# Performance work log

Hardware: AMD Instinct MI355X
Metric: run time of the kernel (lower is better)

## Reference

```python
import jax, jax.numpy as jnp
import numpy as np

N_NODES = 20000
N_INPUT = 64
K_MAX = 12
BITS = 64
N_OUT = 10
BATCH = 64
T = 128


def setup_inputs() -> dict:
    key = jax.random.key(0)
    ks = jax.random.split(key, 8)
    x = jax.random.randint(ks[0], (BATCH, T, BITS), 0, 2, dtype=jnp.int32)
    w_in = jax.random.randint(ks[1], (BITS, N_INPUT), 0, 2, dtype=jnp.int32)
    adj_list = jax.random.randint(ks[2], (N_NODES, K_MAX), 0, N_NODES, dtype=jnp.int32)
    adj_mask = jax.random.randint(ks[3], (N_NODES, K_MAX), 0, 2, dtype=jnp.int32)
    lut = jax.random.randint(ks[4], (N_NODES, 2 ** K_MAX), 0, 2, dtype=jnp.int32)
    init_states = jax.random.randint(ks[5], (1, N_NODES), 0, 2, dtype=jnp.int32)
    W_out = jax.random.normal(ks[6], (N_OUT, N_NODES - N_INPUT), dtype=jnp.float32) * 0.02
    b_out = jnp.zeros((N_OUT,), dtype=jnp.float32)
    return {"x": x, "w_in": w_in, "adj_list": adj_list, "adj_mask": adj_mask,
            "lut": lut, "init_states": init_states, "W_out": W_out, "b_out": b_out}


def reference(x, w_in, adj_list, adj_mask, lut, init_states, W_out, b_out):
    B, T_, bits = x.shape
    N, k = adj_list.shape
    I = w_in.shape[1]
    # powers_of_2, big-endian order as in make_minimal_powers_of_two (flip)
    powers = (2 ** jnp.arange(k - 1, -1, -1)).astype(jnp.int32)  # [k]
    no_neigh = ~(adj_mask.astype(bool).any(axis=1))              # [N] nodes w/o neighbours keep state
    node_ids = jnp.arange(N)
    states0 = jnp.broadcast_to(init_states, (B, N)).astype(jnp.int32)

    def step(states, x_t):
        # inject input: bipartite mapping of input bits onto first I nodes (OR-combine)
        u = ((x_t @ w_in) > 0).astype(jnp.int32)                 # [B, I]
        states = states.at[:, :I].set(u)
        # gather incoming neighbour states per node (irregular gather)
        neigh = jnp.take(states, adj_list, axis=1)               # [B, N, k]
        neigh = neigh * adj_mask[None, :, :]
        # bit-pack into LUT index
        idx = (neigh * powers[None, None, :]).sum(axis=-1)       # [B, N], < 2^k
        new = lut[node_ids[None, :], idx]                        # [B, N] LUT lookup
        new = jnp.where(no_neigh[None, :], states, new)
        return new, None

    states, _ = jax.lax.scan(step, states0, jnp.swapaxes(x, 0, 1))
    # readout on reservoir (non-input) nodes at final timestep
    feats = states[:, I:].astype(jnp.float32)                    # [B, N-I]
    out = jax.nn.sigmoid(feats @ W_out.T + b_out)                # [B, n_outputs]
    return out
```

## Files before the change

kernel.cpp:

```cpp
#include <hip/hip_runtime.h>
#include <cstdint>
#include <cstddef>


#define N_NODES   20000
#define N_INPUT   64
#define K_MAX     12
#define T_STEPS   128
#define N_BATCH   64
#define N_OUT     10
#define N_FEAT    (N_NODES - N_INPUT)
#define DUMMY_NODE 20000
#define ST_WORDS  20004

#define NBLK 512
#define NTHR 512
#define NPB  39
#define NPB_PAD 40
#define BAR_CNT 64
#define GO_CNT  8
#define BAR_STRIDE 32

typedef unsigned long long u64;

__global__ __launch_bounds__(256) void pack_x_kernel(const int* __restrict__ x,
                                                     u64* __restrict__ xp) {
  const int t = blockIdx.x;
  const int wave = threadIdx.x >> 6, lane = threadIdx.x & 63;
  for (int b = wave; b < N_BATCH; b += 4) {
    int v = x[((size_t)b * T_STEPS + t) * 64 + lane];
    u64 bal = __ballot(v != 0);
    if (lane == 0) xp[(size_t)t * N_BATCH + b] = bal;
  }
}

__global__ __launch_bounds__(256) void init_kernel(const int* __restrict__ inis,
                                                   const int* __restrict__ w_in,
                                                   const u64* __restrict__ xp,
                                                   u64* __restrict__ buf0,
                                                   u64* __restrict__ buf1,
                                                   u64* __restrict__ wcol,
                                                   unsigned* __restrict__ bar) {
  if (blockIdx.x < 79) {
    int n = blockIdx.x * 256 + threadIdx.x;
    if (n >= N_INPUT && n < ST_WORDS) {
      u64 w = (n < N_NODES && inis[n] != 0) ? ~0ull : 0ull;
      buf0[n] = w;
      buf1[n] = w;
    }
  } else {
    const int wave = threadIdx.x >> 6, lane = threadIdx.x & 63;
    u64 xw = xp[lane];
    for (int i = wave; i < 64; i += 4) {
      int wv = w_in[(size_t)lane * 64 + i];
      u64 wc = __ballot(wv != 0);
      if (lane == 0) wcol[i] = wc;
      u64 ub = __ballot((xw & wc) != 0);
      if (lane == 0) buf0[i] = ub;
    }
    if (threadIdx.x < BAR_CNT + GO_CNT)
      bar[threadIdx.x * BAR_STRIDE] = 0u;
  }
}

__global__ __launch_bounds__(64) void u_pre_kernel(const u64* __restrict__ xp,
                                                   const u64* __restrict__ wcol,
                                                   u64* __restrict__ u_all) {
  const int t = blockIdx.x, lane = threadIdx.x;
  u64 xw = xp[(size_t)t * N_BATCH + lane];
  for (int i = 0; i < 64; i++) {
    u64 ub = __ballot((xw & wcol[i]) != 0);
    if (lane == 0) u_all[(size_t)t * 64 + i] = ub;
  }
}

__device__ __forceinline__ u64 bit_transpose64(u64 w, int lane) {
  const u64 LO0 = 0x00000000FFFFFFFFull, LO1 = 0x0000FFFF0000FFFFull,
            LO2 = 0x00FF00FF00FF00FFull, LO3 = 0x0F0F0F0F0F0F0F0Full,
            LO4 = 0x3333333333333333ull, LO5 = 0x5555555555555555ull;
#define XP_STAGE(d, LO)                                                  \
  {                                                                      \
    u64 p = (u64)__shfl_xor((long long)w, (d), 64);                      \
    if (lane & (d)) w = ((p >> (d)) & (LO)) | (w & ~(LO));               \
    else            w = (w & (LO)) | ((p << (d)) & ~(LO));               \
  }
  XP_STAGE(32, LO0) XP_STAGE(16, LO1) XP_STAGE(8, LO2)
  XP_STAGE(4,  LO3) XP_STAGE(2,  LO4) XP_STAGE(1, LO5)
#undef XP_STAGE
  return w;
}

__global__ __launch_bounds__(NTHR, 4) void reservoir_kernel(
    const int* __restrict__ lut, const int* __restrict__ adj,
    const int* __restrict__ mask, const u64* __restrict__ u_all,
    u64* __restrict__ buf0, u64* __restrict__ buf1,
    unsigned* __restrict__ bar) {
  __shared__ u64 lut_lds[NPB_PAD * 64];
  __shared__ int adj_lds[NPB_PAD * K_MAX];
  __shared__ unsigned char hn_lds[NPB_PAD];

  const int bi = blockIdx.x;
  const int tid = threadIdx.x;
  const int wave = tid >> 6, lane = tid & 63;
  const int base = N_INPUT + bi * NPB;
  const int nloc = min(NPB, N_NODES - base);

  if (tid < NPB_PAD) {
    int i = tid, h = 0;
    if (i < nloc) {
      for (int j = 0; j < K_MAX; j++) {
        int m = mask[(size_t)(base + i) * K_MAX + j];
        int a = adj[(size_t)(base + i) * K_MAX + j];
        adj_lds[i * K_MAX + (K_MAX - 1 - j)] = m ? a : DUMMY_NODE;
        h |= m;
      }
    } else {
      for (int j = 0; j < K_MAX; j++) adj_lds[i * K_MAX + j] = DUMMY_NODE;
    }
    hn_lds[i] = (unsigned char)(h ? 1 : 0);
  }

  const int nwords = nloc * 64;
  const int* lp = lut + (size_t)base * 4096;
  for (int w0 = wave * 8; w0 < nwords; w0 += 64) {
    int v[8];
#pragma unroll
    for (int q = 0; q < 8; q++) {
      int widx = w0 + q;
      v[q] = (widx < nwords) ? lp[(size_t)widx * 64 + lane] : 0;
    }
#pragma unroll
    for (int q = 0; q < 8; q++) {
      int widx = w0 + q;
      u64 bal = __ballot(v[q] != 0);
      if (lane == 0 && widx < nwords) lut_lds[widx] = bal;
    }
  }
  __syncthreads();

  const int l0 = wave * 5;
  const int cnt = min(5, nloc - l0);

  for (int t = 0; t < T_STEPS; t++) {
    u64* cur = (t & 1) ? buf1 : buf0;
    u64* nxt = (t & 1) ? buf0 : buf1;

    u64 w = 0;
    if (lane < 60) {
      int a = adj_lds[l0 * K_MAX + lane];
      w = __hip_atomic_load(&cur[a], __ATOMIC_RELAXED, __HIP_MEMORY_SCOPE_AGENT);
    }
    w = bit_transpose64(w, lane);

#pragma unroll
    for (int i = 0; i < 5; i++) {
      if (i < cnt) {
        unsigned idx = (unsigned)(w >> (12 * i)) & 0xFFFu;
        u64 g = lut_lds[(l0 + i) * 64 + (idx >> 6)];
        u64 res = __ballot((g >> (idx & 63)) & 1ull);
        if (lane == 0 && hn_lds[l0 + i])
          __hip_atomic_store(&nxt[base + l0 + i], res,
                             __ATOMIC_RELAXED, __HIP_MEMORY_SCOPE_AGENT);
      }
    }

    if (bi == NBLK - 1 && wave == 7 && t + 1 < T_STEPS) {
      u64 uw = u_all[(size_t)(t + 1) * 64 + lane];
      __hip_atomic_store(&nxt[lane], uw, __ATOMIC_RELAXED, __HIP_MEMORY_SCOPE_AGENT);
    }

    if (t != T_STEPS - 1) {
      __syncthreads();
      __builtin_amdgcn_fence(__ATOMIC_RELEASE, "workgroup");
      if (tid == 0)
        __hip_atomic_fetch_add(&bar[(bi & (BAR_CNT - 1)) * BAR_STRIDE], 1u,
                               __ATOMIC_RELAXED, __HIP_MEMORY_SCOPE_AGENT);
      if (bi == 0 && wave == 0) {
        const unsigned tgt = (unsigned)(t + 1) * (NBLK / BAR_CNT);
        for (;;) {
          unsigned c = __hip_atomic_load(&bar[lane * BAR_STRIDE],
                                         __ATOMIC_RELAXED, __HIP_MEMORY_SCOPE_AGENT);
          if (__all(c >= tgt)) break;
          __builtin_amdgcn_s_sleep(2);
        }
        if (lane < GO_CNT)
          __hip_atomic_store(&bar[(BAR_CNT + lane) * BAR_STRIDE], (unsigned)(t + 1),
                             __ATOMIC_RELAXED, __HIP_MEMORY_SCOPE_AGENT);
      } else if (wave == 0) {
        unsigned* gp = &bar[(BAR_CNT + (bi & (GO_CNT - 1))) * BAR_STRIDE];
        while (__hip_atomic_load(gp, __ATOMIC_RELAXED, __HIP_MEMORY_SCOPE_AGENT)
               < (unsigned)(t + 1))
          __builtin_amdgcn_s_sleep(2);
      }
      __builtin_amdgcn_fence(__ATOMIC_ACQUIRE, "workgroup");
      __syncthreads();
    }
  }
}

__global__ __launch_bounds__(256) void readout_kernel(const u64* __restrict__ st,
                                                      const float* __restrict__ Wout,
                                                      const float* __restrict__ bout,
                                                      float* __restrict__ out) {
  const int b = blockIdx.x / N_OUT;
  const int o = blockIdx.x % N_OUT;
  float acc = 0.f;
  for (int n = threadIdx.x; n < N_FEAT; n += 256) {
    u64 s = st[N_INPUT + n];
    float w = Wout[(size_t)o * N_FEAT + n];
    acc += ((s >> b) & 1ull) ? w : 0.f;
  }
  for (int off = 32; off > 0; off >>= 1) acc += __shfl_down(acc, off);
  __shared__ float red[4];
  const int wave = threadIdx.x >> 6, lane = threadIdx.x & 63;
  if (lane == 0) red[wave] = acc;
  __syncthreads();
  if (threadIdx.x == 0) {
    float tot = red[0] + red[1] + red[2] + red[3] + bout[o];
    out[(size_t)b * N_OUT + o] = 1.f / (1.f + __expf(-tot));
  }
}

extern "C" void kernel_launch(void* const* d_in, const int* in_sizes, int n_in,
                              void* d_out, int out_size, void* d_ws, size_t ws_size,
                              hipStream_t stream) {
  const int* x    = (const int*)d_in[0];
  const int* w_in = (const int*)d_in[1];
  const int* adj  = (const int*)d_in[2];
  const int* mask = (const int*)d_in[3];
  const int* lut  = (const int*)d_in[4];
  const int* inis = (const int*)d_in[5];
  const float* Wout = (const float*)d_in[6];
  const float* bout = (const float*)d_in[7];
  float* out = (float*)d_out;

  char* ws = (char*)d_ws;
  size_t off = 0;
  auto alloc = [&](size_t bytes) -> void* {
    void* p = ws + off;
    off += (bytes + 255) & ~(size_t)255;
    return p;
  };
  u64* buf0 = (u64*)alloc((size_t)ST_WORDS * 8);
  u64* buf1 = (u64*)alloc((size_t)ST_WORDS * 8);
  u64* xp   = (u64*)alloc((size_t)T_STEPS * N_BATCH * 8);
  u64* wcol = (u64*)alloc(64 * 8);
  u64* u_all = (u64*)alloc((size_t)T_STEPS * 64 * 8);
  unsigned* bar = (unsigned*)alloc((size_t)(BAR_CNT + GO_CNT) * BAR_STRIDE * 4);
  (void)ws_size; (void)in_sizes; (void)n_in; (void)out_size;

  hipLaunchKernelGGL(pack_x_kernel, dim3(T_STEPS), dim3(256), 0, stream, x, xp);
  hipLaunchKernelGGL(init_kernel, dim3(80), dim3(256), 0, stream,
                     inis, w_in, xp, buf0, buf1, wcol, bar);
  hipLaunchKernelGGL(u_pre_kernel, dim3(T_STEPS), dim3(64), 0, stream,
                     xp, wcol, u_all);

  void* args[] = {(void*)&lut, (void*)&adj, (void*)&mask, (void*)&u_all,
                  (void*)&buf0, (void*)&buf1, (void*)&bar};
  hipLaunchCooperativeKernel((const void*)reservoir_kernel,
                             dim3(NBLK), dim3(NTHR), args, 0, stream);

  hipLaunchKernelGGL(readout_kernel, dim3(N_BATCH * N_OUT), dim3(256), 0, stream,
                     buf0, Wout, bout, out);
}
```

Baseline: 1.033 ms.

## Use fewer, larger blocks with tree barrier and direct input-node reads

Halves the grid to 256 blocks of 1024 threads, each owning 78 nodes. The polling grid barrier, where block 0 spins on 64 counters, becomes a two-level arrival tree: the last arriver at each leaf bumps a root counter, and the last root arriver publishes the go flag. Input-node neighbours are now read straight from the precomputed per-step u_all array, so the last block no longer writes input states into the next buffer. Per-node result stores are merged into a single lane-parallel store per wave. Fewer blocks mean fewer barrier participants, at the cost of a longer serial critical path through the atomics and different occupancy with 1024-thread blocks.

```diff
diff --git a/kernel.cpp b/kernel.cpp
--- a/kernel.cpp
+++ b/kernel.cpp
@@ -13,13 +13,14 @@
 #define DUMMY_NODE 20000
 #define ST_WORDS  20004
 
-#define NBLK 512
-#define NTHR 512
-#define NPB  39
-#define NPB_PAD 40
-#define BAR_CNT 64
+#define NBLK 256
+#define NTHR 1024
+#define NPB  78
+#define NPB_PAD 80
+#define LEAF_CNT 64
 #define GO_CNT  8
 #define BAR_STRIDE 32
+#define ROOT_IDX 64
 
 typedef unsigned long long u64;
 
@@ -36,7 +37,6 @@
 
 __global__ __launch_bounds__(256) void init_kernel(const int* __restrict__ inis,
                                                    const int* __restrict__ w_in,
-                                                   const u64* __restrict__ xp,
                                                    u64* __restrict__ buf0,
                                                    u64* __restrict__ buf1,
                                                    u64* __restrict__ wcol,
@@ -50,15 +50,12 @@
     }
   } else {
     const int wave = threadIdx.x >> 6, lane = threadIdx.x & 63;
-    u64 xw = xp[lane];
     for (int i = wave; i < 64; i += 4) {
       int wv = w_in[(size_t)lane * 64 + i];
       u64 wc = __ballot(wv != 0);
       if (lane == 0) wcol[i] = wc;
-      u64 ub = __ballot((xw & wc) != 0);
-      if (lane == 0) buf0[i] = ub;
-    }
-    if (threadIdx.x < BAR_CNT + GO_CNT)
+    }
+    if (threadIdx.x < ROOT_IDX + 1 + GO_CNT)
       bar[threadIdx.x * BAR_STRIDE] = 0u;
   }
 }
@@ -90,7 +87,7 @@
   return w;
 }
 
-__global__ __launch_bounds__(NTHR, 4) void reservoir_kernel(
+__global__ __launch_bounds__(NTHR) void reservoir_kernel(
     const int* __restrict__ lut, const int* __restrict__ adj,
     const int* __restrict__ mask, const u64* __restrict__ u_all,
     u64* __restrict__ buf0, u64* __restrict__ buf1,
@@ -122,7 +119,7 @@
 
   const int nwords = nloc * 64;
   const int* lp = lut + (size_t)base * 4096;
-  for (int w0 = wave * 8; w0 < nwords; w0 += 64) {
+  for (int w0 = wave * 8; w0 < nwords; w0 += 128) {
     int v[8];
 #pragma unroll
     for (int q = 0; q < 8; q++) {
@@ -140,57 +137,59 @@
 
   const int l0 = wave * 5;
   const int cnt = min(5, nloc - l0);
+  const bool do_store = (lane < cnt) && hn_lds[l0 + lane];
 
   for (int t = 0; t < T_STEPS; t++) {
     u64* cur = (t & 1) ? buf1 : buf0;
     u64* nxt = (t & 1) ? buf0 : buf1;
+    const u64* ubase = u_all + (size_t)t * 64;
 
     u64 w = 0;
     if (lane < 60) {
       int a = adj_lds[l0 * K_MAX + lane];
-      w = __hip_atomic_load(&cur[a], __ATOMIC_RELAXED, __HIP_MEMORY_SCOPE_AGENT);
+      const u64* p = (a < N_INPUT) ? (ubase + a) : (cur + a);
+      w = __hip_atomic_load(p, __ATOMIC_RELAXED, __HIP_MEMORY_SCOPE_AGENT);
     }
     w = bit_transpose64(w, lane);
 
+    u64 keep = 0;
 #pragma unroll
     for (int i = 0; i < 5; i++) {
       if (i < cnt) {
         unsigned idx = (unsigned)(w >> (12 * i)) & 0xFFFu;
         u64 g = lut_lds[(l0 + i) * 64 + (idx >> 6)];
         u64 res = __ballot((g >> (idx & 63)) & 1ull);
-        if (lane == 0 && hn_lds[l0 + i])
-          __hip_atomic_store(&nxt[base + l0 + i], res,
-                             __ATOMIC_RELAXED, __HIP_MEMORY_SCOPE_AGENT);
+        if (lane == i) keep = res;
       }
     }
-
-    if (bi == NBLK - 1 && wave == 7 && t + 1 < T_STEPS) {
-      u64 uw = u_all[(size_t)(t + 1) * 64 + lane];
-      __hip_atomic_store(&nxt[lane], uw, __ATOMIC_RELAXED, __HIP_MEMORY_SCOPE_AGENT);
-    }
+    if (do_store)
+      __hip_atomic_store(&nxt[base + l0 + lane], keep,
+                         __ATOMIC_RELAXED, __HIP_MEMORY_SCOPE_AGENT);
 
     if (t != T_STEPS - 1) {
       __syncthreads();
       __builtin_amdgcn_fence(__ATOMIC_RELEASE, "workgroup");
-      if (tid == 0)
-        __hip_atomic_fetch_add(&bar[(bi & (BAR_CNT - 1)) * BAR_STRIDE], 1u,
+      if (wave == 0) {
+        unsigned leafold = 0;
+        if (lane == 0)
+          leafold = __hip_atomic_fetch_add(&bar[(bi & (LEAF_CNT - 1)) * BAR_STRIDE],
+                                           1u, __ATOMIC_RELAXED, __HIP_MEMORY_SCOPE_AGENT);
+        leafold = (unsigned)__shfl((int)leafold, 0);
+        if (leafold == (unsigned)t * (NBLK / LEAF_CNT) + (NBLK / LEAF_CNT - 1)) {
+          unsigned rootold = 0;
+          if (lane == 0)
+            rootold = __hip_atomic_fetch_add(&bar[ROOT_IDX * BAR_STRIDE], 1u,
+                                             __ATOMIC_RELAXED, __HIP_MEMORY_SCOPE_AGENT);
+          rootold = (unsigned)__shfl((int)rootold, 0);
+          if (rootold == (unsigned)t * LEAF_CNT + (LEAF_CNT - 1) && lane < GO_CNT)
+            __hip_atomic_store(&bar[(ROOT_IDX + 1 + lane) * BAR_STRIDE],
+                               (unsigned)(t + 1),
                                __ATOMIC_RELAXED, __HIP_MEMORY_SCOPE_AGENT);
-      if (bi == 0 && wave == 0) {
-        const unsigned tgt = (unsigned)(t + 1) * (NBLK / BAR_CNT);
-        for (;;) {
-          unsigned c = __hip_atomic_load(&bar[lane * BAR_STRIDE],
-                                         __ATOMIC_RELAXED, __HIP_MEMORY_SCOPE_AGENT);
-          if (__all(c >= tgt)) break;
-          __builtin_amdgcn_s_sleep(2);
         }
-        if (lane < GO_CNT)
-          __hip_atomic_store(&bar[(BAR_CNT + lane) * BAR_STRIDE], (unsigned)(t + 1),
-                             __ATOMIC_RELAXED, __HIP_MEMORY_SCOPE_AGENT);
-      } else if (wave == 0) {
-        unsigned* gp = &bar[(BAR_CNT + (bi & (GO_CNT - 1))) * BAR_STRIDE];
+        unsigned* gp = &bar[(ROOT_IDX + 1 + (bi & (GO_CNT - 1))) * BAR_STRIDE];
         while (__hip_atomic_load(gp, __ATOMIC_RELAXED, __HIP_MEMORY_SCOPE_AGENT)
                < (unsigned)(t + 1))
-          __builtin_amdgcn_s_sleep(2);
+          __builtin_amdgcn_s_sleep(1);
       }
       __builtin_amdgcn_fence(__ATOMIC_ACQUIRE, "workgroup");
       __syncthreads();
@@ -246,12 +245,12 @@
   u64* xp   = (u64*)alloc((size_t)T_STEPS * N_BATCH * 8);
   u64* wcol = (u64*)alloc(64 * 8);
   u64* u_all = (u64*)alloc((size_t)T_STEPS * 64 * 8);
-  unsigned* bar = (unsigned*)alloc((size_t)(BAR_CNT + GO_CNT) * BAR_STRIDE * 4);
+  unsigned* bar = (unsigned*)alloc((size_t)(ROOT_IDX + 1 + GO_CNT) * BAR_STRIDE * 4);
   (void)ws_size; (void)in_sizes; (void)n_in; (void)out_size;
 
   hipLaunchKernelGGL(pack_x_kernel, dim3(T_STEPS), dim3(256), 0, stream, x, xp);
   hipLaunchKernelGGL(init_kernel, dim3(80), dim3(256), 0, stream,
-                     inis, w_in, xp, buf0, buf1, wcol, bar);
+                     inis, w_in, buf0, buf1, wcol, bar);
   hipLaunchKernelGGL(u_pre_kernel, dim3(T_STEPS), dim3(64), 0, stream,
                      xp, wcol, u_all);
 
```

Result: slower. 1.061 ms (+2.7%).
